# Performance work log

Measured on AMD Instinct MI355X. Metric: run time of the kernel, lower is better.

## Reference

```python
import jax, jax.numpy as jnp
import numpy as np

NUM_CHARS = 26  # hardcoded in original module


def setup_inputs() -> dict:
    key = jax.random.key(0)
    ks = jax.random.split(key, 8)
    B, T, H = 2048, 1024, NUM_CHARS
    s = 1.0 / np.sqrt(H)
    return {
        "x": jax.random.randint(ks[0], (B, T), 0, NUM_CHARS, dtype=jnp.int64),
        "E": jax.random.normal(ks[1], (NUM_CHARS, H), dtype=jnp.float32),            # embedding table
        "W_ih": jax.random.uniform(ks[2], (4 * H, H), jnp.float32, -s, s),           # LSTM input weights (i,f,g,o)
        "W_hh": jax.random.uniform(ks[3], (4 * H, H), jnp.float32, -s, s),           # LSTM hidden weights
        "b_ih": jax.random.uniform(ks[4], (4 * H,), jnp.float32, -s, s),
        "b_hh": jax.random.uniform(ks[5], (4 * H,), jnp.float32, -s, s),
        "W_lin": jax.random.uniform(ks[6], (NUM_CHARS, H), jnp.float32, -s, s),      # final Linear weight
        "b_lin": jax.random.uniform(ks[7], (NUM_CHARS,), jnp.float32, -s, s),
    }


def reference(x, E, W_ih, W_hh, b_ih, b_hh, W_lin, b_lin):
    # Embedding lookup: [B,T] -> [B,T,H]
    emb = E[x]
    B, T, H = emb.shape
    # Precompute input projections for all timesteps: [B,T,4H]
    x_proj = jnp.einsum('bth,gh->btg', emb, W_ih) + b_ih

    def step(carry, xt):  # xt: [B,4H]
        h, c = carry
        gates = xt + h @ W_hh.T + b_hh  # [B,4H], torch gate order i,f,g,o
        i, f, g, o = jnp.split(gates, 4, axis=-1)
        i = jax.nn.sigmoid(i)
        f = jax.nn.sigmoid(f)
        g = jnp.tanh(g)
        o = jax.nn.sigmoid(o)
        c = f * c + i * g
        h = o * jnp.tanh(c)
        return (h, c), None

    h0 = jnp.zeros((B, H), emb.dtype)
    (hT, _), _ = jax.lax.scan(step, (h0, h0), jnp.swapaxes(x_proj, 0, 1))
    # h_n has shape [num_layers=1, B, H]; .squeeze(1) is a no-op for B>1
    out = hT @ W_lin.T + b_lin  # [B,26]
    return out[None]  # [1,B,26]
```

## Files before the change

kernel.cpp:

```cpp
#include <hip/hip_runtime.h>

#define LOG2E 1.442695040888963f

typedef float f32x2 __attribute__((ext_vector_type(2)));
typedef float f32x4 __attribute__((ext_vector_type(4)));

static __device__ __forceinline__ void pkfma(f32x2& acc, f32x2 a, f32x2 b) {
    asm("v_pk_fma_f32 %0, %1, %2, %0" : "+v"(acc) : "v"(a), "v"(b));
}
static __device__ __forceinline__ void pkmul(f32x2& d, f32x2 a, f32x2 b) {
    asm("v_pk_mul_f32 %0, %1, %2" : "=v"(d) : "v"(a), "v"(b));
}

__launch_bounds__(64, 2)
__global__ void lstm_char_kernel(const int* __restrict__ x,
                                 const float* __restrict__ E,
                                 const float* __restrict__ W_ih,
                                 const float* __restrict__ W_hh,
                                 const float* __restrict__ b_ih,
                                 const float* __restrict__ b_hh,
                                 const float* __restrict__ W_lin,
                                 const float* __restrict__ b_lin,
                                 float* __restrict__ out,
                                 int T)
{
    constexpr int H = 26;

    __shared__ __align__(16) f32x2 P[27][52];
    __shared__ float Ebuf[676];
    __shared__ int   chars[1026];
    __shared__ __align__(16) float hbuf[64];

    const int b = blockIdx.x;
    const int l = threadIdx.x;
    const bool act = (l < 52);
    const int r0 = act ? l : 0;
    const int r1 = act ? l + 52 : 0;

    for (int i = l; i < 676; i += 64) Ebuf[i] = E[i];
    for (int t = l; t < T; t += 64) chars[t] = x[(size_t)b * T + t] * 416;
    if (l < 2) chars[1024 + l] = 0;
    hbuf[l] = 0.0f;

    const float m0 = -LOG2E;
    const float m1 = (l < 26) ? (-2.0f * LOG2E) : (-LOG2E);
    const float s1 = (l < 26) ? 2.0f : 1.0f;
    const float d1 = (l < 26) ? -1.0f : 0.0f;

    f32x2 wh0p[13], wh1p[13];
    #pragma unroll
    for (int k = 0; k < 13; ++k) {
        wh0p[k] = f32x2{W_hh[r0 * H + 2 * k] * m0, W_hh[r0 * H + 2 * k + 1] * m0};
        wh1p[k] = f32x2{W_hh[r1 * H + 2 * k] * m1, W_hh[r1 * H + 2 * k + 1] * m1};
    }

    {
        float wi0[H], wi1[H];
        #pragma unroll
        for (int k = 0; k < H; ++k) {
            wi0[k] = W_ih[r0 * H + k];
            wi1[k] = W_ih[r1 * H + k];
        }
        const float bias0 = b_ih[r0] + b_hh[r0];
        const float bias1 = b_ih[r1] + b_hh[r1];
        __syncthreads();
        for (int ch = 0; ch < 26; ++ch) {
            float a0 = bias0, a1 = bias1;
            #pragma unroll
            for (int k = 0; k < H; ++k) {
                float e = Ebuf[ch * H + k];
                a0 = fmaf(wi0[k], e, a0);
                a1 = fmaf(wi1[k], e, a1);
            }
            if (act) P[ch][l] = f32x2{a0 * m0, a1 * m1};
        }
    }
    __syncthreads();

    const int bpaddr = ((l - 26) & 63) << 2;
    const int hidx   = (l - 26) & 63;
    const char* Pb = (const char*)&P[0][0];
    const int lane8 = l << 3;

    int poffn = chars[1];
    f32x2 pa = *(const f32x2*)(Pb + chars[0] + lane8);
    float c = 0.0f;

    #pragma unroll 2
    for (int t = 0; t < T; ++t) {
        f32x2 hp[13];
        #pragma unroll
        for (int q = 0; q < 13; ++q) hp[q] = ((const f32x2*)hbuf)[q];

        f32x2 pn = *(const f32x2*)(Pb + poffn + lane8);
        int poff2 = chars[t + 2];

        f32x2 A0, A1, B0, B1;
        pkmul(A0, wh0p[0], hp[0]);
        pkmul(A1, wh0p[1], hp[1]);
        pkmul(B0, wh1p[0], hp[0]);
        pkmul(B1, wh1p[1], hp[1]);
        #pragma unroll
        for (int k = 2; k < 12; k += 2) {
            pkfma(A0, wh0p[k],     hp[k]);
            pkfma(A1, wh0p[k + 1], hp[k + 1]);
            pkfma(B0, wh1p[k],     hp[k]);
            pkfma(B1, wh1p[k + 1], hp[k + 1]);
        }
        pkfma(A0, wh0p[12], hp[12]);
        pkfma(B0, wh1p[12], hp[12]);
        f32x2 sa = A0 + A1;
        f32x2 sb = B0 + B1;
        const float a0s = sa.x + sa.y + pa.x;
        const float a1s = sb.x + sb.y + pa.y;

        float y0 = __builtin_amdgcn_rcpf(1.0f + __builtin_amdgcn_exp2f(a0s));
        float y1 = fmaf(__builtin_amdgcn_rcpf(1.0f + __builtin_amdgcn_exp2f(a1s)),
                        s1, d1);

        float pr = y0 * y1;
        float pp = __int_as_float(
            __builtin_amdgcn_ds_bpermute(bpaddr, __float_as_int(pr)));

        c = fmaf(y0, c, pp);
        float th = fmaf(__builtin_amdgcn_rcpf(
                            1.0f + __builtin_amdgcn_exp2f(c * (-2.0f * LOG2E))),
                        2.0f, -1.0f);
        hbuf[hidx] = y1 * th;

        pa = pn; poffn = poff2;
    }

    __syncthreads();

    if (l < H) {
        float acc = b_lin[l];
        #pragma unroll
        for (int k = 0; k < H; ++k)
            acc = fmaf(W_lin[l * H + k], hbuf[k], acc);
        out[(size_t)b * H + l] = acc;
    }
}

extern "C" void kernel_launch(void* const* d_in, const int* in_sizes, int n_in,
                              void* d_out, int out_size, void* d_ws, size_t ws_size,
                              hipStream_t stream) {
    const int*   x     = (const int*)d_in[0];
    const float* E     = (const float*)d_in[1];
    const float* W_ih  = (const float*)d_in[2];
    const float* W_hh  = (const float*)d_in[3];
    const float* b_ih  = (const float*)d_in[4];
    const float* b_hh  = (const float*)d_in[5];
    const float* W_lin = (const float*)d_in[6];
    const float* b_lin = (const float*)d_in[7];
    float* out = (float*)d_out;

    const int T = 1024;
    const int B = in_sizes[0] / T;

    lstm_char_kernel<<<B, 64, 0, stream>>>(x, E, W_ih, W_hh, b_ih, b_hh,
                                           W_lin, b_lin, out, T);
}
```

Before: 282.3 us.

## Realign gate lanes to 32-lane halves and use permlane32 swap

Gate rows are remapped so each 32-lane half of the wave holds one gate pair, with 6 lanes per half left idle. The cross-lane exchange of i*g into the forget/cell lanes then uses v_permlane32_swap in place of ds_bpermute, which avoids an LDS-path permute on the serial recurrence. The cell state is kept pre-scaled by -2*log2e so the tanh needs one fewer multiply, h is loaded with 128-bit reads, and packed FMA operand order is swapped. The cost is a wider, padded P table and more arithmetic folded into the scale constants, which is a numerical-correctness risk.

```diff
diff --git a/kernel.cpp b/kernel.cpp
--- a/kernel.cpp
+++ b/kernel.cpp
@@ -26,26 +26,28 @@
 {
     constexpr int H = 26;
 
-    __shared__ __align__(16) f32x2 P[27][52];
+    __shared__ __align__(16) f32x2 P[26][64];
     __shared__ float Ebuf[676];
     __shared__ int   chars[1026];
     __shared__ __align__(16) float hbuf[64];
 
     const int b = blockIdx.x;
     const int l = threadIdx.x;
-    const bool act = (l < 52);
-    const int r0 = act ? l : 0;
-    const int r1 = act ? l + 52 : 0;
+    const int j = l & 31;
+    const bool lo = (l < 32);
+    const int rr = (j < 26) ? j : 0;
+    const int r0 = lo ? rr : 26 + rr;
+    const int r1 = lo ? 52 + rr : 78 + rr;
 
     for (int i = l; i < 676; i += 64) Ebuf[i] = E[i];
-    for (int t = l; t < T; t += 64) chars[t] = x[(size_t)b * T + t] * 416;
+    for (int t = l; t < T; t += 64) chars[t] = x[(size_t)b * T + t] * 512;
     if (l < 2) chars[1024 + l] = 0;
     hbuf[l] = 0.0f;
 
     const float m0 = -LOG2E;
-    const float m1 = (l < 26) ? (-2.0f * LOG2E) : (-LOG2E);
-    const float s1 = (l < 26) ? 2.0f : 1.0f;
-    const float d1 = (l < 26) ? -1.0f : 0.0f;
+    const float m1 = lo ? (-2.0f * LOG2E) : (-LOG2E);
+    const float s1 = lo ? (-4.0f * LOG2E) : 1.0f;
+    const float d1 = lo ? ( 2.0f * LOG2E) : 0.0f;
 
     f32x2 wh0p[13], wh1p[13];
     #pragma unroll
@@ -72,43 +74,49 @@
                 a0 = fmaf(wi0[k], e, a0);
                 a1 = fmaf(wi1[k], e, a1);
             }
-            if (act) P[ch][l] = f32x2{a0 * m0, a1 * m1};
+            P[ch][l] = f32x2{a0 * m0, a1 * m1};
         }
     }
     __syncthreads();
 
-    const int bpaddr = ((l - 26) & 63) << 2;
-    const int hidx   = (l - 26) & 63;
+    const int hidx = (l - 32) & 63;
     const char* Pb = (const char*)&P[0][0];
     const int lane8 = l << 3;
 
     int poffn = chars[1];
     f32x2 pa = *(const f32x2*)(Pb + chars[0] + lane8);
-    float c = 0.0f;
+    float C = 0.0f;
 
     #pragma unroll 2
     for (int t = 0; t < T; ++t) {
+        f32x4 hv4[7];
+        #pragma unroll
+        for (int q = 0; q < 7; ++q) hv4[q] = ((const f32x4*)hbuf)[q];
         f32x2 hp[13];
         #pragma unroll
-        for (int q = 0; q < 13; ++q) hp[q] = ((const f32x2*)hbuf)[q];
+        for (int q = 0; q < 6; ++q) {
+            hp[2 * q]     = f32x2{hv4[q].x, hv4[q].y};
+            hp[2 * q + 1] = f32x2{hv4[q].z, hv4[q].w};
+        }
+        hp[12] = f32x2{hv4[6].x, hv4[6].y};
 
         f32x2 pn = *(const f32x2*)(Pb + poffn + lane8);
         int poff2 = chars[t + 2];
 
         f32x2 A0, A1, B0, B1;
-        pkmul(A0, wh0p[0], hp[0]);
-        pkmul(A1, wh0p[1], hp[1]);
-        pkmul(B0, wh1p[0], hp[0]);
-        pkmul(B1, wh1p[1], hp[1]);
+        pkmul(A0, hp[0], wh0p[0]);
+        pkmul(A1, hp[1], wh0p[1]);
+        pkmul(B0, hp[0], wh1p[0]);
+        pkmul(B1, hp[1], wh1p[1]);
         #pragma unroll
         for (int k = 2; k < 12; k += 2) {
-            pkfma(A0, wh0p[k],     hp[k]);
-            pkfma(A1, wh0p[k + 1], hp[k + 1]);
-            pkfma(B0, wh1p[k],     hp[k]);
-            pkfma(B1, wh1p[k + 1], hp[k + 1]);
+            pkfma(A0, hp[k],     wh0p[k]);
+            pkfma(A1, hp[k + 1], wh0p[k + 1]);
+            pkfma(B0, hp[k],     wh1p[k]);
+            pkfma(B1, hp[k + 1], wh1p[k + 1]);
         }
-        pkfma(A0, wh0p[12], hp[12]);
-        pkfma(B0, wh1p[12], hp[12]);
+        pkfma(A0, hp[12], wh0p[12]);
+        pkfma(B0, hp[12], wh1p[12]);
         f32x2 sa = A0 + A1;
         f32x2 sb = B0 + B1;
         const float a0s = sa.x + sa.y + pa.x;
@@ -117,16 +125,19 @@
         float y0 = __builtin_amdgcn_rcpf(1.0f + __builtin_amdgcn_exp2f(a0s));
         float y1 = fmaf(__builtin_amdgcn_rcpf(1.0f + __builtin_amdgcn_exp2f(a1s)),
                         s1, d1);
+        float y1_2 = y1 + y1;
+        float ny1  = -y1;
 
         float pr = y0 * y1;
-        float pp = __int_as_float(
-            __builtin_amdgcn_ds_bpermute(bpaddr, __float_as_int(pr)));
+        auto sw = __builtin_amdgcn_permlane32_swap(__float_as_int(pr),
+                                                   __float_as_int(pr),
+                                                   false, false);
+        float rcv = (__int_as_float(sw[0]) + __int_as_float(sw[1])) - pr;
 
-        c = fmaf(y0, c, pp);
-        float th = fmaf(__builtin_amdgcn_rcpf(
-                            1.0f + __builtin_amdgcn_exp2f(c * (-2.0f * LOG2E))),
-                        2.0f, -1.0f);
-        hbuf[hidx] = y1 * th;
+        C = fmaf(y0, C, rcv);
+        float rc = __builtin_amdgcn_rcpf(1.0f + __builtin_amdgcn_exp2f(C));
+        float hv = fmaf(rc, y1_2, ny1);
+        hbuf[hidx] = hv;
 
         pa = pn; poffn = poff2;
     }
```

Result: no change. 285.1 us (+1.0%).
